# Performance work log

Measured on AMD Instinct MI355X. Metric: run time of the kernel, lower is better.

Reference implementation:

```python
import jax, jax.numpy as jnp
import numpy as np

NUM_SLOTS = 8
ITERS = 3
EPS = 1e-8
LN_EPS = 1e-5
B, N, D = 64, 4096, 128
H = 256


def _ln(x, w, b):
    m = jnp.mean(x, axis=-1, keepdims=True)
    v = jnp.mean(jnp.square(x - m), axis=-1, keepdims=True)
    return (x - m) * jax.lax.rsqrt(v + LN_EPS) * w + b


def setup_inputs() -> dict:
    key = jax.random.key(0)
    ks = jax.random.split(key, 10)
    s = 0.02
    return {
        "inputs": jax.random.normal(ks[0], (B, N, D), jnp.float32),
        "noise": jax.random.normal(ks[1], (B, NUM_SLOTS, D), jnp.float32),
        "ln_in_w": jnp.ones((D,), jnp.float32), "ln_in_b": jnp.zeros((D,), jnp.float32),
        "ln_s_w": jnp.ones((D,), jnp.float32), "ln_s_b": jnp.zeros((D,), jnp.float32),
        "ln_m_w": jnp.ones((D,), jnp.float32), "ln_m_b": jnp.zeros((D,), jnp.float32),
        "slot_mu": jnp.zeros((1, 1, D), jnp.float32),
        "slot_sigma": jnp.ones((1, 1, D), jnp.float32),
        "Wq": s * jax.random.normal(ks[2], (D, D), jnp.float32),
        "Wk": s * jax.random.normal(ks[3], (D, D), jnp.float32),
        "Wv": s * jax.random.normal(ks[4], (D, D), jnp.float32),
        "W_ih": s * jax.random.normal(ks[5], (3 * D, D), jnp.float32),
        "W_hh": s * jax.random.normal(ks[6], (3 * D, D), jnp.float32),
        "b_ih": jnp.zeros((3 * D,), jnp.float32), "b_hh": jnp.zeros((3 * D,), jnp.float32),
        "W1": s * jax.random.normal(ks[7], (H, D), jnp.float32), "b1": jnp.zeros((H,), jnp.float32),
        "W2": s * jax.random.normal(ks[8], (D, H), jnp.float32), "b2": jnp.zeros((D,), jnp.float32),
    }


def reference(inputs, noise, ln_in_w, ln_in_b, ln_s_w, ln_s_b, ln_m_w, ln_m_b,
              slot_mu, slot_sigma, Wq, Wk, Wv, W_ih, W_hh, b_ih, b_hh, W1, b1, W2, b2):
    b, n, d = inputs.shape
    x = _ln(inputs, ln_in_w, ln_in_b)
    sigma = jax.nn.softplus(slot_sigma)
    slots = slot_mu + sigma * noise  # [b, S, d]
    k = jnp.einsum('bnd,ed->bne', x, Wk)
    v = jnp.einsum('bnd,ed->bne', x, Wv)
    scale = 1.0 / jnp.sqrt(jnp.asarray(d, inputs.dtype))
    for _ in range(ITERS):
        slots_prev = slots
        q = jnp.einsum('bsd,ed->bse', _ln(slots, ln_s_w, ln_s_b), Wq)
        dots = jnp.einsum('bne,bse->bns', k, q) * scale  # [b, n, S]
        attn = jax.nn.softmax(dots, axis=-1) + EPS       # softmax over slots
        attn = attn / jnp.sum(attn, axis=-2, keepdims=True)  # normalize over inputs
        updates = jnp.einsum('bns,bnd->bsd', attn, v)
        # GRUCell: input=updates, hidden=slots_prev
        gi = jnp.einsum('bsd,ed->bse', updates, W_ih) + b_ih      # [b,S,3d]
        gh = jnp.einsum('bsd,ed->bse', slots_prev, W_hh) + b_hh
        i_r, i_z, i_n = jnp.split(gi, 3, axis=-1)
        h_r, h_z, h_n = jnp.split(gh, 3, axis=-1)
        r = jax.nn.sigmoid(i_r + h_r)
        z = jax.nn.sigmoid(i_z + h_z)
        nn_ = jnp.tanh(i_n + r * h_n)
        slots = (1.0 - z) * nn_ + z * slots_prev
    h = jax.nn.relu(jnp.einsum('bsd,hd->bsh', _ln(slots, ln_m_w, ln_m_b), W1) + b1)
    slots = slots + jnp.einsum('bsh,dh->bsd', h, W2) + b2
    return slots
```

## Files before the change

kernel.cpp:

```cpp
#include <hip/hip_runtime.h>
#include <math.h>

#define NB 64
#define NN 4096
#define ND 128
#define NS 8
#define NH 256
#define CHUNKS 16
#define ROWS_PER_CHUNK 256

static constexpr float EPSA  = 1e-8f;
static constexpr float LNE   = 1e-5f;
static constexpr float SCALE = 0.08838834764831845f;

#define OFF_SLOTS 0
#define OFF_QK    65536
#define OFF_WC    131072
#define OFF_M2T   180224
#define OFF_QKB   196608
#define OFF_PART  196736
#define OFF_PCS   1245312

__device__ __forceinline__ float dot4f(float4 a, float4 b) {
    return fmaf(a.x, b.x, fmaf(a.y, b.y, fmaf(a.z, b.z, a.w * b.w)));
}

__global__ __launch_bounds__(256) void prep_kernel(
    const float* __restrict__ noise, const float* __restrict__ ln_s_w,
    const float* __restrict__ ln_s_b, const float* __restrict__ slot_mu,
    const float* __restrict__ slot_sigma, const float* __restrict__ Wq,
    const float* __restrict__ Wk, const float* __restrict__ Wv,
    const float* __restrict__ W_ih, float* __restrict__ ws)
{
    int bid = blockIdx.x, t = threadIdx.x;
    if (bid < 32) {
        int i0 = (bid * 256 + t) * 8;
        int d0 = i0 & 127;
        float o[8];
#pragma unroll
        for (int j = 0; j < 8; j++) {
            float sg = slot_sigma[d0 + j];
            float sp = fmaxf(sg, 0.f) + log1pf(expf(-fabsf(sg)));
            o[j] = fmaf(sp, noise[i0 + j], slot_mu[d0 + j]);
        }
        float4* dst = (float4*)(ws + OFF_SLOTS + i0);
        dst[0] = make_float4(o[0], o[1], o[2], o[3]);
        dst[1] = make_float4(o[4], o[5], o[6], o[7]);
    } else if (bid < 224) {
        int g = (bid - 32) * 2 + (t >> 7);
        int f = t & 127;
        const float* wih = W_ih + g * ND;
        float acc = 0.f;
        for (int e = 0; e < ND; e++) acc = fmaf(wih[e], Wv[e * ND + f], acc);
        ws[OFF_WC + g * ND + f] = acc;
    } else {
        int dp = (bid - 224) * 2 + (t >> 7);
        int d = t & 127;
        float acc = 0.f;
        for (int e = 0; e < ND; e++) acc = fmaf(Wq[e * ND + d], Wk[e * ND + dp], acc);
        ws[OFF_M2T + dp * ND + d] = SCALE * ln_s_w[d] * acc;
        float c = ln_s_b[d] * acc;
#pragma unroll
        for (int m = 1; m <= 32; m <<= 1) c += __shfl_xor(c, m, 64);
        __shared__ float red[4];
        if ((t & 63) == 0) red[t >> 6] = c;
        __syncthreads();
        if (t == 0)   ws[OFF_QKB + dp] = SCALE * (red[0] + red[1]);
        if (t == 128) ws[OFF_QKB + dp] = SCALE * (red[2] + red[3]);
    }
}

__global__ __launch_bounds__(512) void qk0_kernel(float* __restrict__ ws)
{
    __shared__ float sh_s[NS * ND];
    __shared__ float sh_ln[NS * ND];
    int b = blockIdx.x, t = threadIdx.x;
    sh_s[t]       = ws[OFF_SLOTS + b * NS * ND + t];
    sh_s[t + 512] = ws[OFF_SLOTS + b * NS * ND + t + 512];
    __syncthreads();
    {
        int wid = t >> 6, l = t & 63;
        float v0 = sh_s[wid * ND + 2 * l], v1 = sh_s[wid * ND + 2 * l + 1];
        float s1 = v0 + v1, s2 = fmaf(v0, v0, v1 * v1);
#pragma unroll
        for (int m = 1; m <= 32; m <<= 1) { s1 += __shfl_xor(s1, m, 64); s2 += __shfl_xor(s2, m, 64); }
        float mean = s1 * (1.f / 128.f);
        float var = fmaf(-mean, mean, s2 * (1.f / 128.f));
        float tv = var + LNE;
        float rs = rsqrtf(tv); rs = rs * (1.5f - 0.5f * tv * rs * rs);
        sh_ln[wid * ND + 2 * l]     = (v0 - mean) * rs;
        sh_ln[wid * ND + 2 * l + 1] = (v1 - mean) * rs;
    }
    __syncthreads();
    {
        int g = t >> 3, c = t & 7, s = g >> 3, dp0 = g & 7;
        const float4* lp = (const float4*)(sh_ln + s * ND + c * 16);
        float4 l0 = lp[0], l1 = lp[1], l2 = lp[2], l3 = lp[3];
#pragma unroll 2
        for (int j = 0; j < 16; j++) {
            int dp = dp0 + 8 * j;
            const float4* m4 = (const float4*)(ws + OFF_M2T + dp * ND + c * 16);
            float a = dot4f(m4[0], l0) + dot4f(m4[1], l1) + dot4f(m4[2], l2) + dot4f(m4[3], l3);
            a += __shfl_xor(a, 1); a += __shfl_xor(a, 2); a += __shfl_xor(a, 4);
            if (c == 0) ws[OFF_QK + b * NS * ND + s * ND + dp] = a + ws[OFF_QKB + dp];
        }
    }
}

__global__ __launch_bounds__(256) void attn_kernel(
    const float* __restrict__ inp, const float* __restrict__ lnw,
    const float* __restrict__ lnb, float* __restrict__ ws)
{
    __shared__ float qk_lds[NS * ND];
    __shared__ float red_lds[4][NS][ND];
    __shared__ float cs_lds[4][NS];
    int t = threadIdx.x;
    int b = blockIdx.x >> 4, chunk = blockIdx.x & 15;
    int w = t >> 6, lane = t & 63;
    int rg = lane >> 4, colg = lane & 15;

    {
        const float4* src = (const float4*)(ws + OFF_QK + b * NS * ND);
        ((float4*)qk_lds)[t] = src[t];
    }
    float wv[8], bv[8];
    {
        const float4* w4 = (const float4*)(lnw + colg * 8);
        const float4* b4 = (const float4*)(lnb + colg * 8);
        float4 wa = w4[0], wb = w4[1], ba = b4[0], bb = b4[1];
        wv[0]=wa.x; wv[1]=wa.y; wv[2]=wa.z; wv[3]=wa.w; wv[4]=wb.x; wv[5]=wb.y; wv[6]=wb.z; wv[7]=wb.w;
        bv[0]=ba.x; bv[1]=ba.y; bv[2]=ba.z; bv[3]=ba.w; bv[4]=bb.x; bv[5]=bb.y; bv[6]=bb.z; bv[7]=bb.w;
    }
    float acc[NS][8];
    float cs[NS];
#pragma unroll
    for (int si = 0; si < NS; si++) {
        cs[si] = 0.f;
#pragma unroll
        for (int j = 0; j < 8; j++) acc[si][j] = 0.f;
    }
    __syncthreads();

    const float* base = inp + ((size_t)b * NN + chunk * ROWS_PER_CHUNK + w * 64 + rg) * ND + colg * 8;
#pragma unroll 2
    for (int q = 0; q < 16; q++) {
        const float* rp = base + q * 4 * ND;
        float4 a0 = *(const float4*)rp;
        float4 a1 = *(const float4*)(rp + 4);
        float x[8] = {a0.x, a0.y, a0.z, a0.w, a1.x, a1.y, a1.z, a1.w};
        float s1 = 0.f, s2 = 0.f;
#pragma unroll
        for (int j = 0; j < 8; j++) { s1 += x[j]; s2 = fmaf(x[j], x[j], s2); }
#pragma unroll
        for (int m = 1; m <= 8; m <<= 1) { s1 += __shfl_xor(s1, m, 64); s2 += __shfl_xor(s2, m, 64); }
        float mean = s1 * (1.f / 128.f);
        float var = fmaf(-mean, mean, s2 * (1.f / 128.f));
        float tv = var + LNE;
        float rs = rsqrtf(tv); rs = rs * (1.5f - 0.5f * tv * rs * rs);
#pragma unroll
        for (int j = 0; j < 8; j++) x[j] = fmaf((x[j] - mean) * rs, wv[j], bv[j]);

        float pd[NS];
#pragma unroll
        for (int si = 0; si < NS; si++) {
            const float4* q4 = (const float4*)(qk_lds + si * ND + colg * 8);
            float4 q0 = q4[0], q1 = q4[1];
            float p = x[0] * q0.x;
            p = fmaf(x[1], q0.y, p); p = fmaf(x[2], q0.z, p); p = fmaf(x[3], q0.w, p);
            p = fmaf(x[4], q1.x, p); p = fmaf(x[5], q1.y, p); p = fmaf(x[6], q1.z, p);
            p = fmaf(x[7], q1.w, p);
            pd[si] = p;
        }
#pragma unroll
        for (int m = 1; m <= 8; m <<= 1) {
#pragma unroll
            for (int si = 0; si < NS; si++) pd[si] += __shfl_xor(pd[si], m, 64);
        }
        float mx = fmaxf(fmaxf(fmaxf(pd[0], pd[1]), fmaxf(pd[2], pd[3])),
                         fmaxf(fmaxf(pd[4], pd[5]), fmaxf(pd[6], pd[7])));
        float ev[NS]; float es = 0.f;
#pragma unroll
        for (int si = 0; si < NS; si++) { ev[si] = __expf(pd[si] - mx); es += ev[si]; }
        float r0 = __builtin_amdgcn_rcpf(es);
        float inv = r0 * (2.0f - es * r0);
#pragma unroll
        for (int si = 0; si < NS; si++) {
            float p = ev[si] * inv;
            cs[si] += p;
#pragma unroll
            for (int j = 0; j < 8; j++) acc[si][j] = fmaf(p, x[j], acc[si][j]);
        }
    }
#pragma unroll
    for (int m = 16; m <= 32; m <<= 1) {
#pragma unroll
        for (int si = 0; si < NS; si++) {
            cs[si] += __shfl_xor(cs[si], m, 64);
#pragma unroll
            for (int j = 0; j < 8; j++) acc[si][j] += __shfl_xor(acc[si][j], m, 64);
        }
    }
    if (lane < 16) {
#pragma unroll
        for (int si = 0; si < NS; si++) {
            *(float4*)&red_lds[w][si][lane * 8]     = make_float4(acc[si][0], acc[si][1], acc[si][2], acc[si][3]);
            *(float4*)&red_lds[w][si][lane * 8 + 4] = make_float4(acc[si][4], acc[si][5], acc[si][6], acc[si][7]);
        }
    }
    if (lane == 0) {
#pragma unroll
        for (int si = 0; si < NS; si++) cs_lds[w][si] = cs[si];
    }
    __syncthreads();
    float* pout = ws + OFF_PART + (size_t)(b * CHUNKS + chunk) * (NS * ND);
#pragma unroll
    for (int k = 0; k < 4; k++) {
        int o = t + k * 256;
        pout[o] = red_lds[0][0][o] + red_lds[1][0][o] + red_lds[2][0][o] + red_lds[3][0][o];
    }
    if (t < NS) {
        ws[OFF_PCS + (b * CHUNKS + chunk) * NS + t] =
            cs_lds[0][t] + cs_lds[1][t] + cs_lds[2][t] + cs_lds[3][t];
    }
}

template <int LAST>
__global__ __launch_bounds__(512) void gru_kernel(
    const float* __restrict__ W_hh, const float* __restrict__ b_ih,
    const float* __restrict__ b_hh, const float* __restrict__ W1,
    const float* __restrict__ b1, const float* __restrict__ W2,
    const float* __restrict__ b2, const float* __restrict__ ln_m_w,
    const float* __restrict__ ln_m_b, float* __restrict__ ws,
    float* __restrict__ out)
{
    __shared__ float sh_nr[4 * ND];
    __shared__ float sh_sp[4 * ND];
    __shared__ float sh_tmp[512];
    __shared__ float sh_sx[ND];
    __shared__ float sh_cs[4];
    __shared__ float sh_gi[4 * 384];
    __shared__ float sh_gh[4 * 384];
    __shared__ float sh_ln[4 * ND];
    int b = blockIdx.x >> 1, sh2 = blockIdx.x & 1;
    int t = threadIdx.x;

    const float* partf = ws + OFF_PART + (size_t)b * CHUNKS * NS * ND;
    {
        float r = 0.f;
#pragma unroll
        for (int p = 0; p < CHUNKS; p++) r += partf[p * 1024 + sh2 * 512 + t];
        sh_nr[t] = r;
    }
    {
        int e = t & 127, q = t >> 7;
        float a = 0.f;
#pragma unroll
        for (int p = q * 4; p < q * 4 + 4; p++)
#pragma unroll
            for (int s = 0; s < 8; s++) a += partf[p * 1024 + s * 128 + e];
        sh_tmp[t] = a;
    }
    if (t < 4) {
        const float* pcs = ws + OFF_PCS + b * CHUNKS * NS;
        float c = 0.f;
#pragma unroll
        for (int p = 0; p < CHUNKS; p++) c += pcs[p * NS + sh2 * 4 + t];
        sh_cs[t] = c + (float)NN * EPSA;
    }
    sh_sp[t] = ws[OFF_SLOTS + b * NS * ND + sh2 * 512 + t];
    __syncthreads();
    if (t < ND) sh_sx[t] = sh_tmp[t] + sh_tmp[t + 128] + sh_tmp[t + 256] + sh_tmp[t + 384];
    __syncthreads();
    sh_nr[t] = fmaf(EPSA, sh_sx[t & 127], sh_nr[t]) / sh_cs[t >> 7];
    __syncthreads();
    int g = t >> 3, c = t & 7;
    int sl = g >> 4, g3 = g & 15;
    {
        const float4* np = (const float4*)(sh_nr + sl * ND + c * 16);
        const float4* pp = (const float4*)(sh_sp + sl * ND + c * 16);
        float4 n0 = np[0], n1 = np[1], n2 = np[2], n3 = np[3];
        float4 p0 = pp[0], p1 = pp[1], p2 = pp[2], p3 = pp[3];
#pragma unroll 2
        for (int j = 0; j < 24; j++) {
            int e3 = g3 + 16 * j;
            const float4* wc4 = (const float4*)(ws + OFF_WC + e3 * ND + c * 16);
            const float4* wh4 = (const float4*)(W_hh + e3 * ND + c * 16);
            float ai = dot4f(wc4[0], n0) + dot4f(wc4[1], n1) + dot4f(wc4[2], n2) + dot4f(wc4[3], n3);
            float ah = dot4f(wh4[0], p0) + dot4f(wh4[1], p1) + dot4f(wh4[2], p2) + dot4f(wh4[3], p3);
            ai += __shfl_xor(ai, 1); ah += __shfl_xor(ah, 1);
            ai += __shfl_xor(ai, 2); ah += __shfl_xor(ah, 2);
            ai += __shfl_xor(ai, 4); ah += __shfl_xor(ah, 4);
            if (c == 0) {
                sh_gi[sl * 384 + e3] = ai + b_ih[e3];
                sh_gh[sl * 384 + e3] = ah + b_hh[e3];
            }
        }
    }
    __syncthreads();
    {
        int si = t >> 7, d = t & 127;
        float gir = sh_gi[si * 384 + d],       ghr = sh_gh[si * 384 + d];
        float giz = sh_gi[si * 384 + 128 + d], ghz = sh_gh[si * 384 + 128 + d];
        float gin = sh_gi[si * 384 + 256 + d], ghn = sh_gh[si * 384 + 256 + d];
        float rr = 1.f / (1.f + expf(-(gir + ghr)));
        float z  = 1.f / (1.f + expf(-(giz + ghz)));
        float nn_ = tanhf(fmaf(rr, ghn, gin));
        float ns = fmaf(z, sh_sp[t] - nn_, nn_);
        sh_nr[t] = ns;
        if (!LAST) ws[OFF_SLOTS + b * NS * ND + sh2 * 512 + t] = ns;
    }
    __syncthreads();
    {
        int wid = t >> 6, l = t & 63;
        if (wid < 4) {
            float v0 = sh_nr[wid * ND + 2 * l], v1 = sh_nr[wid * ND + 2 * l + 1];
            float s1 = v0 + v1, s2 = fmaf(v0, v0, v1 * v1);
#pragma unroll
            for (int m = 1; m <= 32; m <<= 1) { s1 += __shfl_xor(s1, m, 64); s2 += __shfl_xor(s2, m, 64); }
            float mean = s1 * (1.f / 128.f);
            float var = fmaf(-mean, mean, s2 * (1.f / 128.f));
            float tv = var + LNE;
            float rs = rsqrtf(tv); rs = rs * (1.5f - 0.5f * tv * rs * rs);
            float x0 = (v0 - mean) * rs, x1 = (v1 - mean) * rs;
            if (LAST) {
                x0 = fmaf(x0, ln_m_w[2 * l],     ln_m_b[2 * l]);
                x1 = fmaf(x1, ln_m_w[2 * l + 1], ln_m_b[2 * l + 1]);
            }
            sh_ln[wid * ND + 2 * l]     = x0;
            sh_ln[wid * ND + 2 * l + 1] = x1;
        }
    }
    __syncthreads();
    if (!LAST) {
        const float4* lp = (const float4*)(sh_ln + sl * ND + c * 16);
        float4 l0 = lp[0], l1 = lp[1], l2 = lp[2], l3 = lp[3];
#pragma unroll 2
        for (int j = 0; j < 8; j++) {
            int dp = g3 + 16 * j;
            const float4* m4 = (const float4*)(ws + OFF_M2T + dp * ND + c * 16);
            float a = dot4f(m4[0], l0) + dot4f(m4[1], l1) + dot4f(m4[2], l2) + dot4f(m4[3], l3);
            a += __shfl_xor(a, 1); a += __shfl_xor(a, 2); a += __shfl_xor(a, 4);
            if (c == 0) ws[OFF_QK + b * NS * ND + (sh2 * 4 + sl) * ND + dp] = a + ws[OFF_QKB + dp];
        }
    } else {
        const float4* lp = (const float4*)(sh_ln + sl * ND + c * 16);
        float4 l0 = lp[0], l1 = lp[1], l2 = lp[2], l3 = lp[3];
#pragma unroll 2
        for (int j = 0; j < 16; j++) {
            int hh = g3 + 16 * j;
            const float4* w14 = (const float4*)(W1 + hh * ND + c * 16);
            float a = dot4f(w14[0], l0) + dot4f(w14[1], l1) + dot4f(w14[2], l2) + dot4f(w14[3], l3);
            a += __shfl_xor(a, 1); a += __shfl_xor(a, 2); a += __shfl_xor(a, 4);
            if (c == 0) sh_gi[sl * NH + hh] = fmaxf(a + b1[hh], 0.f);
        }
        __syncthreads();
        const float4* hp = (const float4*)(sh_gi + sl * NH + c * 32);
        float4 h0 = hp[0], h1 = hp[1], h2 = hp[2], h3 = hp[3];
        float4 h4 = hp[4], h5 = hp[5], h6 = hp[6], h7 = hp[7];
#pragma unroll 2
        for (int j = 0; j < 8; j++) {
            int d = g3 + 16 * j;
            const float4* w24 = (const float4*)(W2 + d * NH + c * 32);
            float a = dot4f(w24[0], h0) + dot4f(w24[1], h1) + dot4f(w24[2], h2) + dot4f(w24[3], h3)
                    + dot4f(w24[4], h4) + dot4f(w24[5], h5) + dot4f(w24[6], h6) + dot4f(w24[7], h7);
            a += __shfl_xor(a, 1); a += __shfl_xor(a, 2); a += __shfl_xor(a, 4);
            if (c == 0) out[(size_t)b * NS * ND + (sh2 * 4 + sl) * ND + d] = a + b2[d] + sh_nr[sl * ND + d];
        }
    }
}

extern "C" void kernel_launch(void* const* d_in, const int* in_sizes, int n_in,
                              void* d_out, int out_size, void* d_ws, size_t ws_size,
                              hipStream_t stream) {
    (void)in_sizes; (void)n_in; (void)out_size; (void)ws_size;
    const float* inputs     = (const float*)d_in[0];
    const float* noise      = (const float*)d_in[1];
    const float* ln_in_w    = (const float*)d_in[2];
    const float* ln_in_b    = (const float*)d_in[3];
    const float* ln_s_w     = (const float*)d_in[4];
    const float* ln_s_b     = (const float*)d_in[5];
    const float* ln_m_w     = (const float*)d_in[6];
    const float* ln_m_b     = (const float*)d_in[7];
    const float* slot_mu    = (const float*)d_in[8];
    const float* slot_sigma = (const float*)d_in[9];
    const float* Wq         = (const float*)d_in[10];
    const float* Wk         = (const float*)d_in[11];
    const float* Wv         = (const float*)d_in[12];
    const float* W_ih       = (const float*)d_in[13];
    const float* W_hh       = (const float*)d_in[14];
    const float* b_ih       = (const float*)d_in[15];
    const float* b_hh       = (const float*)d_in[16];
    const float* W1         = (const float*)d_in[17];
    const float* b1         = (const float*)d_in[18];
    const float* W2         = (const float*)d_in[19];
    const float* b2         = (const float*)d_in[20];
    float* ws  = (float*)d_ws;
    float* out = (float*)d_out;

    hipLaunchKernelGGL(prep_kernel, dim3(288), dim3(256), 0, stream,
                       noise, ln_s_w, ln_s_b, slot_mu, slot_sigma, Wq, Wk, Wv, W_ih, ws);
    hipLaunchKernelGGL(qk0_kernel, dim3(NB), dim3(512), 0, stream, ws);
    for (int it = 0; it < 3; ++it) {
        hipLaunchKernelGGL(attn_kernel, dim3(NB * CHUNKS), dim3(256), 0, stream,
                           inputs, ln_in_w, ln_in_b, ws);
        if (it < 2) {
            hipLaunchKernelGGL((gru_kernel<0>), dim3(NB * 2), dim3(512), 0, stream,
                               W_hh, b_ih, b_hh, W1, b1, W2, b2, ln_m_w, ln_m_b, ws, out);
        } else {
            hipLaunchKernelGGL((gru_kernel<1>), dim3(NB * 2), dim3(512), 0, stream,
                               W_hh, b_ih, b_hh, W1, b1, W2, b2, ln_m_w, ln_m_b, ws, out);
        }
    }
}
```

Baseline: 484.8 us.

## Use DPP lane reductions and split partial-sum reduction into separate kernel

Replaces the `__shfl_xor` butterfly reductions with DPP-based adds. These cover quad permutes plus the row half-mirror and row mirror, across 8 and 16 lanes, and avoid LDS-routed cross-lane traffic in the attention inner loop and the GEMV-style loops. It adds a `reduce_kernel` that sums the per-chunk partial updates and column sums over 512 blocks, so the 128-block GRU kernel no longer serially reads all 16 partial chunks. It also adds an occupancy hint to `attn_kernel` and raises an unroll factor. The cost is one extra launch per iteration and an extra workspace round trip for the reduced updates.

```diff
diff --git a/kernel.cpp b/kernel.cpp
--- a/kernel.cpp
+++ b/kernel.cpp
@@ -18,11 +18,28 @@
 #define OFF_WC    131072
 #define OFF_M2T   180224
 #define OFF_QKB   196608
-#define OFF_PART  196736
-#define OFF_PCS   1245312
+#define OFF_UPD   196736
+#define OFF_CS    262272
+#define OFF_PART  262784
+#define OFF_PCS   1311360
 
 __device__ __forceinline__ float dot4f(float4 a, float4 b) {
     return fmaf(a.x, b.x, fmaf(a.y, b.y, fmaf(a.z, b.z, a.w * b.w)));
+}
+
+template <int CTRL>
+__device__ __forceinline__ float dpp_radd(float v) {
+    return v + __int_as_float(__builtin_amdgcn_update_dpp(
+        __float_as_int(v), __float_as_int(v), CTRL, 0xF, 0xF, false));
+}
+__device__ __forceinline__ float red16(float v) {
+    v = dpp_radd<0xB1>(v); v = dpp_radd<0x4E>(v);
+    v = dpp_radd<0x141>(v); v = dpp_radd<0x140>(v);
+    return v;
+}
+__device__ __forceinline__ float red8(float v) {
+    v = dpp_radd<0xB1>(v); v = dpp_radd<0x4E>(v); v = dpp_radd<0x141>(v);
+    return v;
 }
 
 __global__ __launch_bounds__(256) void prep_kernel(
@@ -101,13 +118,13 @@
             int dp = dp0 + 8 * j;
             const float4* m4 = (const float4*)(ws + OFF_M2T + dp * ND + c * 16);
             float a = dot4f(m4[0], l0) + dot4f(m4[1], l1) + dot4f(m4[2], l2) + dot4f(m4[3], l3);
-            a += __shfl_xor(a, 1); a += __shfl_xor(a, 2); a += __shfl_xor(a, 4);
+            a = red8(a);
             if (c == 0) ws[OFF_QK + b * NS * ND + s * ND + dp] = a + ws[OFF_QKB + dp];
         }
     }
 }
 
-__global__ __launch_bounds__(256) void attn_kernel(
+__global__ __launch_bounds__(256, 4) void attn_kernel(
     const float* __restrict__ inp, const float* __restrict__ lnw,
     const float* __restrict__ lnb, float* __restrict__ ws)
 {
@@ -151,8 +168,7 @@
         float s1 = 0.f, s2 = 0.f;
 #pragma unroll
         for (int j = 0; j < 8; j++) { s1 += x[j]; s2 = fmaf(x[j], x[j], s2); }
-#pragma unroll
-        for (int m = 1; m <= 8; m <<= 1) { s1 += __shfl_xor(s1, m, 64); s2 += __shfl_xor(s2, m, 64); }
+        s1 = red16(s1); s2 = red16(s2);
         float mean = s1 * (1.f / 128.f);
         float var = fmaf(-mean, mean, s2 * (1.f / 128.f));
         float tv = var + LNE;
@@ -169,12 +185,7 @@
             p = fmaf(x[1], q0.y, p); p = fmaf(x[2], q0.z, p); p = fmaf(x[3], q0.w, p);
             p = fmaf(x[4], q1.x, p); p = fmaf(x[5], q1.y, p); p = fmaf(x[6], q1.z, p);
             p = fmaf(x[7], q1.w, p);
-            pd[si] = p;
-        }
-#pragma unroll
-        for (int m = 1; m <= 8; m <<= 1) {
-#pragma unroll
-            for (int si = 0; si < NS; si++) pd[si] += __shfl_xor(pd[si], m, 64);
+            pd[si] = red16(p);
         }
         float mx = fmaxf(fmaxf(fmaxf(pd[0], pd[1]), fmaxf(pd[2], pd[3])),
                          fmaxf(fmaxf(pd[4], pd[5]), fmaxf(pd[6], pd[7])));
@@ -221,6 +232,21 @@
     if (t < NS) {
         ws[OFF_PCS + (b * CHUNKS + chunk) * NS + t] =
             cs_lds[0][t] + cs_lds[1][t] + cs_lds[2][t] + cs_lds[3][t];
+    }
+}
+
+__global__ __launch_bounds__(128) void reduce_kernel(float* __restrict__ ws)
+{
+    int b = blockIdx.x >> 3, s = blockIdx.x & 7, t = threadIdx.x;
+    const float* part = ws + OFF_PART + (size_t)b * CHUNKS * NS * ND + s * ND;
+    float r = 0.f;
+#pragma unroll
+    for (int p = 0; p < CHUNKS; p++) r += part[p * (NS * ND) + t];
+    ws[OFF_UPD + (b * NS + s) * ND + t] = r;
+    if (t < 16) {
+        float c = ws[OFF_PCS + (b * CHUNKS + t) * NS + s];
+        c = red16(c);
+        if (t == 0) ws[OFF_CS + b * NS + s] = c;
     }
 }
 
@@ -235,7 +261,6 @@
 {
     __shared__ float sh_nr[4 * ND];
     __shared__ float sh_sp[4 * ND];
-    __shared__ float sh_tmp[512];
     __shared__ float sh_sx[ND];
     __shared__ float sh_cs[4];
     __shared__ float sh_gi[4 * 384];
@@ -244,34 +269,17 @@
     int b = blockIdx.x >> 1, sh2 = blockIdx.x & 1;
     int t = threadIdx.x;
 
-    const float* partf = ws + OFF_PART + (size_t)b * CHUNKS * NS * ND;
-    {
-        float r = 0.f;
-#pragma unroll
-        for (int p = 0; p < CHUNKS; p++) r += partf[p * 1024 + sh2 * 512 + t];
-        sh_nr[t] = r;
-    }
-    {
-        int e = t & 127, q = t >> 7;
+    float r = ws[OFF_UPD + b * NS * ND + sh2 * 512 + t];
+    sh_sp[t] = ws[OFF_SLOTS + b * NS * ND + sh2 * 512 + t];
+    if (t < ND) {
         float a = 0.f;
 #pragma unroll
-        for (int p = q * 4; p < q * 4 + 4; p++)
-#pragma unroll
-            for (int s = 0; s < 8; s++) a += partf[p * 1024 + s * 128 + e];
-        sh_tmp[t] = a;
-    }
-    if (t < 4) {
-        const float* pcs = ws + OFF_PCS + b * CHUNKS * NS;
-        float c = 0.f;
-#pragma unroll
-        for (int p = 0; p < CHUNKS; p++) c += pcs[p * NS + sh2 * 4 + t];
-        sh_cs[t] = c + (float)NN * EPSA;
-    }
-    sh_sp[t] = ws[OFF_SLOTS + b * NS * ND + sh2 * 512 + t];
-    __syncthreads();
-    if (t < ND) sh_sx[t] = sh_tmp[t] + sh_tmp[t + 128] + sh_tmp[t + 256] + sh_tmp[t + 384];
-    __syncthreads();
-    sh_nr[t] = fmaf(EPSA, sh_sx[t & 127], sh_nr[t]) / sh_cs[t >> 7];
+        for (int s = 0; s < NS; s++) a += ws[OFF_UPD + b * NS * ND + s * ND + t];
+        sh_sx[t] = a;
+    }
+    if (t < 4) sh_cs[t] = ws[OFF_CS + b * NS + sh2 * 4 + t] + (float)NN * EPSA;
+    __syncthreads();
+    sh_nr[t] = fmaf(EPSA, sh_sx[t & 127], r) / sh_cs[t >> 7];
     __syncthreads();
     int g = t >> 3, c = t & 7;
     int sl = g >> 4, g3 = g & 15;
@@ -280,16 +288,14 @@
         const float4* pp = (const float4*)(sh_sp + sl * ND + c * 16);
         float4 n0 = np[0], n1 = np[1], n2 = np[2], n3 = np[3];
         float4 p0 = pp[0], p1 = pp[1], p2 = pp[2], p3 = pp[3];
-#pragma unroll 2
+#pragma unroll 4
         for (int j = 0; j < 24; j++) {
             int e3 = g3 + 16 * j;
             const float4* wc4 = (const float4*)(ws + OFF_WC + e3 * ND + c * 16);
             const float4* wh4 = (const float4*)(W_hh + e3 * ND + c * 16);
             float ai = dot4f(wc4[0], n0) + dot4f(wc4[1], n1) + dot4f(wc4[2], n2) + dot4f(wc4[3], n3);
             float ah = dot4f(wh4[0], p0) + dot4f(wh4[1], p1) + dot4f(wh4[2], p2) + dot4f(wh4[3], p3);
-            ai += __shfl_xor(ai, 1); ah += __shfl_xor(ah, 1);
-            ai += __shfl_xor(ai, 2); ah += __shfl_xor(ah, 2);
-            ai += __shfl_xor(ai, 4); ah += __shfl_xor(ah, 4);
+            ai = red8(ai); ah = red8(ah);
             if (c == 0) {
                 sh_gi[sl * 384 + e3] = ai + b_ih[e3];
                 sh_gh[sl * 384 + e3] = ah + b_hh[e3];
@@ -339,7 +345,7 @@
             int dp = g3 + 16 * j;
             const float4* m4 = (const float4*)(ws + OFF_M2T + dp * ND + c * 16);
             float a = dot4f(m4[0], l0) + dot4f(m4[1], l1) + dot4f(m4[2], l2) + dot4f(m4[3], l3);
-            a += __shfl_xor(a, 1); a += __shfl_xor(a, 2); a += __shfl_xor(a, 4);
+            a = red8(a);
             if (c == 0) ws[OFF_QK + b * NS * ND + (sh2 * 4 + sl) * ND + dp] = a + ws[OFF_QKB + dp];
         }
     } else {
@@ -350,7 +356,7 @@
             int hh = g3 + 16 * j;
             const float4* w14 = (const float4*)(W1 + hh * ND + c * 16);
             float a = dot4f(w14[0], l0) + dot4f(w14[1], l1) + dot4f(w14[2], l2) + dot4f(w14[3], l3);
-            a += __shfl_xor(a, 1); a += __shfl_xor(a, 2); a += __shfl_xor(a, 4);
+            a = red8(a);
             if (c == 0) sh_gi[sl * NH + hh] = fmaxf(a + b1[hh], 0.f);
         }
         __syncthreads();
@@ -363,7 +369,7 @@
             const float4* w24 = (const float4*)(W2 + d * NH + c * 32);
             float a = dot4f(w24[0], h0) + dot4f(w24[1], h1) + dot4f(w24[2], h2) + dot4f(w24[3], h3)
                     + dot4f(w24[4], h4) + dot4f(w24[5], h5) + dot4f(w24[6], h6) + dot4f(w24[7], h7);
-            a += __shfl_xor(a, 1); a += __shfl_xor(a, 2); a += __shfl_xor(a, 4);
+            a = red8(a);
             if (c == 0) out[(size_t)b * NS * ND + (sh2 * 4 + sl) * ND + d] = a + b2[d] + sh_nr[sl * ND + d];
         }
     }
@@ -403,6 +409,7 @@
     for (int it = 0; it < 3; ++it) {
         hipLaunchKernelGGL(attn_kernel, dim3(NB * CHUNKS), dim3(256), 0, stream,
                            inputs, ln_in_w, ln_in_b, ws);
+        hipLaunchKernelGGL(reduce_kernel, dim3(NB * NS), dim3(128), 0, stream, ws);
         if (it < 2) {
             hipLaunchKernelGGL((gru_kernel<0>), dim3(NB * 2), dim3(512), 0, stream,
                                W_hh, b_ih, b_hh, W1, b1, W2, b2, ln_m_w, ln_m_b, ws, out);
```

Result: slower. 1.637 ms (+237.7%).
